# Optimization experiments

Hardware: AMD Instinct MI355X
Metric: run time of the kernel (lower is better)

Reference implementation:

```python
import jax, jax.numpy as jnp
import numpy as np

B, T, D, H, E, K = 8, 1024, 1024, 16, 8, 2
HS = D // H  # head size
LN_EPS = 1e-5


def setup_inputs() -> dict:
    key = jax.random.key(0)
    ks = jax.random.split(key, 12)
    s = 0.02
    return {
        "x":  jax.random.normal(ks[0], (B, T, D), jnp.float32),
        "Wq": jax.random.normal(ks[1], (H, D, HS), jnp.float32) * s,
        "Wk": jax.random.normal(ks[2], (H, D, HS), jnp.float32) * s,
        "Wv": jax.random.normal(ks[3], (H, D, HS), jnp.float32) * s,
        "Wg": jax.random.normal(ks[4], (D, E), jnp.float32) * s,
        "W1": jax.random.normal(ks[5], (E, D, 4 * D), jnp.float32) * s,
        "b1": jnp.zeros((E, 4 * D), jnp.float32),
        "W2": jax.random.normal(ks[6], (E, 4 * D, D), jnp.float32) * s,
        "b2": jnp.zeros((E, D), jnp.float32),
        "g1": jnp.ones((D,), jnp.float32),
        "be1": jnp.zeros((D,), jnp.float32),
        "g2": jnp.ones((D,), jnp.float32),
        "be2": jnp.zeros((D,), jnp.float32),
    }


def _layernorm(h, g, b):
    mu = jnp.mean(h, axis=-1, keepdims=True)
    var = jnp.mean(jnp.square(h - mu), axis=-1, keepdims=True)
    return (h - mu) * jax.lax.rsqrt(var + LN_EPS) * g + b


def _attention(x, Wq, Wk, Wv):
    # per-head projections (no bias)
    q = jnp.einsum('btd,hde->bhte', x, Wq)
    k = jnp.einsum('btd,hde->bhte', x, Wk)
    v = jnp.einsum('btd,hde->bhte', x, Wv)
    # NOTE: original scales by C**-0.5 where C = x.shape[-1] = n_embed
    scores = jnp.einsum('bhte,bhse->bhts', q, k) * (D ** -0.5)
    causal = jnp.tril(jnp.ones((T, T), bool))
    scores = jnp.where(causal, scores, -jnp.inf)
    attn = jax.nn.softmax(scores, axis=-1)  # dropout = identity (eval)
    out = jnp.einsum('bhts,bhse->bhte', attn, v)
    # concat heads: [B,H,T,HS] -> [B,T,H*HS]
    return out.transpose(0, 2, 1, 3).reshape(B, T, D)


def _moe(x, Wg, W1, b1, W2, b2):
    xs = x.reshape(-1, D)                       # [N, D]
    logits = xs @ Wg                            # [N, E]
    w, sel = jax.lax.top_k(logits, K)           # [N, K]
    w = jax.nn.softmax(w.astype(jnp.float32), axis=-1).astype(x.dtype)
    # combine per-token per-expert weight: [N, E]
    we = jnp.sum(w[..., None] * (sel[..., None] == jnp.arange(E)), axis=1)
    res = jnp.zeros_like(xs)
    for e in range(E):  # fixed small expert count
        h = jax.nn.relu(xs @ W1[e] + b1[e])     # [N, 4D]
        y = h @ W2[e] + b2[e]                   # [N, D]
        res = res + we[:, e:e + 1] * y
    return res.reshape(x.shape)


def reference(x, Wq, Wk, Wv, Wg, W1, b1, W2, b2, g1, be1, g2, be2):
    out = x + _layernorm(_attention(x, Wq, Wk, Wv), g1, be1)
    out = out + _layernorm(_moe(x, Wg, W1, b1, W2, b2), g2, be2)
    return out
```

## Files before the change

### kernel.cpp

```cpp
#include <hip/hip_runtime.h>

#define B_    8
#define T_    1024
#define D_    1024
#define H_    16
#define HS_   64
#define E_    8
#define DFF   4096
#define NTOK  8192
#define NROW  16384

typedef unsigned short u16;
typedef unsigned int   u32;
typedef __attribute__((ext_vector_type(8))) short bf8;
typedef __attribute__((ext_vector_type(4))) float f4;

__device__ __forceinline__ u16 f2bf(float f) {
  u32 u = __float_as_uint(f);
  u32 r = (u + 0x7FFFu + ((u >> 16) & 1u)) >> 16;
  return (u16)r;
}
__device__ __forceinline__ float bf2f(u16 h) {
  return __uint_as_float(((u32)h) << 16);
}

__device__ __forceinline__ f4 mfma16(bf8 a, bf8 b, f4 c) {
  return __builtin_amdgcn_mfma_f32_16x16x32_bf16(a, b, c, 0, 0, 0);
}

typedef const __attribute__((address_space(1))) void* gas_ptr;
typedef __attribute__((address_space(3))) void* las_ptr;
__device__ __forceinline__ void async16(const void* g, void* l) {
  __builtin_amdgcn_global_load_lds((gas_ptr)g, (las_ptr)l, 16, 0, 0);
}

__global__ __launch_bounds__(256) void cvt_x_kernel(const float* __restrict__ x,
                                                    u16* __restrict__ xbf) {
  int i = blockIdx.x * 256 + threadIdx.x;
  float4 v = ((const float4*)x)[i];
  ushort4 o;
  o.x = f2bf(v.x); o.y = f2bf(v.y); o.z = f2bf(v.z); o.w = f2bf(v.w);
  ((ushort4*)xbf)[i] = o;
}

__global__ __launch_bounds__(256) void transpose_cvt_kernel(
    const float* __restrict__ src, u16* __restrict__ dst,
    int R, int C, size_t sStride, size_t dStride) {
  __shared__ float t[32][33];
  src += (size_t)blockIdx.z * sStride;
  dst += (size_t)blockIdx.z * dStride;
  int r0 = blockIdx.x * 32, c0 = blockIdx.y * 32;
  int tx = threadIdx.x & 31, ty = threadIdx.x >> 5;
#pragma unroll
  for (int i = 0; i < 32; i += 8)
    t[ty + i][tx] = src[(size_t)(r0 + ty + i) * C + (c0 + tx)];
  __syncthreads();
#pragma unroll
  for (int i = 0; i < 32; i += 8)
    dst[(size_t)(c0 + ty + i) * R + (r0 + tx)] = f2bf(t[tx][ty + i]);
}

__global__ __launch_bounds__(256) void vtrans_kernel(const u16* __restrict__ qkv,
                                                     u16* __restrict__ Vt) {
  __shared__ u16 t[32][33];
  int bh = blockIdx.z, b = bh >> 4, h = bh & 15;
  const u16* Vg = qkv + (size_t)(32 + h) * NTOK * HS_ + (size_t)b * T_ * HS_;
  u16* Vp = Vt + (size_t)bh * HS_ * T_;
  int t0 = blockIdx.x * 32, c0 = blockIdx.y * 32;
  int tx = threadIdx.x & 31, ty = threadIdx.x >> 5;
#pragma unroll
  for (int i = 0; i < 32; i += 8)
    t[ty + i][tx] = Vg[(size_t)(t0 + ty + i) * HS_ + c0 + tx];
  __syncthreads();
#pragma unroll
  for (int i = 0; i < 32; i += 8)
    Vp[(size_t)(c0 + ty + i) * T_ + t0 + tx] = t[tx][ty + i];
}

__global__ __launch_bounds__(256) void gating_kernel(
    const float* __restrict__ x, const float* __restrict__ Wg,
    int* __restrict__ sel, float* __restrict__ wgt) {
  int wave = threadIdx.x >> 6, lane = threadIdx.x & 63;
  int t = blockIdx.x * 4 + wave;
  int e = lane & 7, grp = lane >> 3;
  const float* xr = x + (size_t)t * D_;
  float acc = 0.f;
  for (int i = 0; i < 128; ++i) {
    int d = grp + i * 8;
    acc += xr[d] * Wg[d * 8 + e];
  }
  acc += __shfl_xor(acc, 8);
  acc += __shfl_xor(acc, 16);
  acc += __shfl_xor(acc, 32);
  float lg[8];
#pragma unroll
  for (int j = 0; j < 8; ++j) lg[j] = __shfl(acc, j);
  int s0 = 0; float v0 = lg[0];
#pragma unroll
  for (int j = 1; j < 8; ++j) if (lg[j] > v0) { v0 = lg[j]; s0 = j; }
  int s1 = -1; float v1 = -3.4e38f;
#pragma unroll
  for (int j = 0; j < 8; ++j) if (j != s0 && lg[j] > v1) { v1 = lg[j]; s1 = j; }
  if (lane == 0) {
    float dd = __expf(v1 - v0);
    float w0 = 1.f / (1.f + dd);
    sel[2 * t]     = s0; sel[2 * t + 1] = s1;
    wgt[2 * t]     = w0; wgt[2 * t + 1] = dd * w0;
  }
}

__global__ __launch_bounds__(256) void offsets_kernel(const int* __restrict__ sel,
                                                      int* __restrict__ meta) {
  __shared__ int hist[E_];
  int tid = threadIdx.x;
  if (tid < E_) hist[tid] = 0;
  __syncthreads();
  for (int i = tid; i < NROW; i += 256) atomicAdd(&hist[sel[i]], 1);
  __syncthreads();
  if (tid == 0) {
    int s = 0, mb = 0;
    for (int e = 0; e < E_; ++e) {
      int c = hist[e];
      meta[e] = c; meta[8 + e] = s; meta[16 + e] = mb;
      s += c; mb += (c + 127) >> 7;
    }
    meta[24] = mb;
  }
}

__global__ __launch_bounds__(256) void assign_kernel(
    const int* __restrict__ sel, const float* __restrict__ wgt,
    const int* __restrict__ meta, int* __restrict__ gidx,
    float* __restrict__ gw, int* __restrict__ rowmap) {
  int e = blockIdx.x, tid = threadIdx.x, lane = tid & 63, wv = tid >> 6;
  __shared__ int wsum[4];
  __shared__ int carry;
  if (tid == 0) carry = meta[8 + e];
  __syncthreads();
  for (int base = 0; base < NROW; base += 256) {
    int idx = base + tid;
    int f = (sel[idx] == e) ? 1 : 0;
    unsigned long long mask = __ballot(f);
    int pre = __popcll(mask & ((1ull << lane) - 1ull));
    if (lane == 0) wsum[wv] = __popcll(mask);
    __syncthreads();
    int woff = 0;
    for (int w = 0; w < wv; ++w) woff += wsum[w];
    int cb = carry;
    if (f) {
      int pos = cb + woff + pre;
      gidx[pos] = idx >> 1;
      gw[pos] = wgt[idx];
      rowmap[idx] = pos;
    }
    __syncthreads();
    if (tid == 0) carry = cb + wsum[0] + wsum[1] + wsum[2] + wsum[3];
    __syncthreads();
  }
}

template <int MODE>
__global__ __launch_bounds__(256) void gemm_bt(
    const u16* __restrict__ A, const u16* __restrict__ Bt,
    u16* __restrict__ outB, const float* __restrict__ bias,
    const int* __restrict__ meta, const int* __restrict__ gidx, int K) {
  int n0 = blockIdx.y * 128;
  int n_e = 0, off = 0, m0, e = 0;
  const u16* Ap = A;
  const u16* Bp = Bt;
  if constexpr (MODE != 0) {
    int xb = blockIdx.x;
#pragma unroll
    for (int j = 1; j < 8; ++j) if (meta[16 + j] <= xb) e = j;
    n_e = meta[e];
    off = meta[8 + e];
    m0 = (xb - meta[16 + e]) * 128;
    if (m0 >= n_e) return;
    if constexpr (MODE == 1) {
      Bp = Bt + (size_t)e * DFF * 1024;
    } else {
      Ap = A + (size_t)off * DFF;
      Bp = Bt + (size_t)e * 1024 * DFF;
    }
  } else {
    m0 = blockIdx.x * 128;
  }

  __shared__ __align__(16) u16 As[128 * 64];
  __shared__ __align__(16) u16 Bs[128 * 64];
  int tid = threadIdx.x, lane = tid & 63, wave = tid >> 6;
  int wm = wave >> 1, wn = wave & 1, ml = lane & 15, quad = lane >> 4;
  int lrow = lane >> 3;
  int gcol = ((lane & 7) ^ lrow) * 8;

  const u16* arow[4];
  const u16* brow[4];
#pragma unroll
  for (int r = 0; r < 4; ++r) {
    int row = wave * 32 + r * 8;
    int ra = m0 + row + lrow;
    if constexpr (MODE == 1) {
      int rr = ra < n_e ? ra : n_e - 1;
      arow[r] = Ap + (size_t)gidx[off + rr] * 1024 + gcol;
    } else if constexpr (MODE == 2) {
      int rr = ra < n_e ? ra : n_e - 1;
      arow[r] = Ap + (size_t)rr * DFF + gcol;
    } else {
      arow[r] = Ap + (size_t)ra * 1024 + gcol;
    }
    brow[r] = Bp + (size_t)(n0 + row + lrow) * K + gcol;
  }

  f4 acc[4][4];
#pragma unroll
  for (int i = 0; i < 4; ++i)
#pragma unroll
    for (int j = 0; j < 4; ++j) acc[i][j] = (f4){0.f, 0.f, 0.f, 0.f};

  int mlx = ml & 7;
  for (int k0 = 0; k0 < K; k0 += 64) {
    __syncthreads();
#pragma unroll
    for (int r = 0; r < 4; ++r) {
      int row = wave * 32 + r * 8;
      async16(arow[r] + k0, &As[row * 64]);
      async16(brow[r] + k0, &Bs[row * 64]);
    }
    __syncthreads();
#pragma unroll
    for (int kk = 0; kk < 64; kk += 32) {
      int p = (((kk >> 3) + quad) ^ mlx) * 8;
      bf8 af[4], bfr[4];
#pragma unroll
      for (int mi = 0; mi < 4; ++mi)
        af[mi] = *(const bf8*)&As[(wm * 64 + mi * 16 + ml) * 64 + p];
#pragma unroll
      for (int ni = 0; ni < 4; ++ni)
        bfr[ni] = *(const bf8*)&Bs[(wn * 64 + ni * 16 + ml) * 64 + p];
#pragma unroll
      for (int mi = 0; mi < 4; ++mi)
#pragma unroll
        for (int ni = 0; ni < 4; ++ni)
          acc[mi][ni] = mfma16(af[mi], bfr[ni], acc[mi][ni]);
    }
  }

#pragma unroll
  for (int mi = 0; mi < 4; ++mi)
#pragma unroll
    for (int ni = 0; ni < 4; ++ni)
#pragma unroll
      for (int rg = 0; rg < 4; ++rg) {
        int m = m0 + wm * 64 + mi * 16 + quad * 4 + rg;
        int n = n0 + wn * 64 + ni * 16 + ml;
        float v = acc[mi][ni][rg];
        if constexpr (MODE == 0) {
          int pl = n >> 6, col = n & 63;
          outB[(size_t)pl * NTOK * HS_ + (size_t)m * HS_ + col] = f2bf(v);
        } else if constexpr (MODE == 1) {
          if (m < n_e) {
            float hv = v + bias[e * DFF + n];
            outB[(size_t)(off + m) * DFF + n] = f2bf(fmaxf(hv, 0.f));
          }
        } else {
          if (m < n_e) {
            outB[(size_t)(off + m) * 1024 + n] = f2bf(v + bias[e * 1024 + n]);
          }
        }
      }
}

__global__ __launch_bounds__(256) void attn_kernel(const u16* __restrict__ qkv,
                                                   const u16* __restrict__ Vt,
                                                   float* __restrict__ attn_out) {
  int qt = blockIdx.x, bh = blockIdx.y;
  int b = bh >> 4, h = bh & 15;
  int q0 = qt * 64;
  const u16* Qg = qkv + (size_t)h * NTOK * HS_ + (size_t)b * T_ * HS_;
  const u16* Kg = qkv + (size_t)(16 + h) * NTOK * HS_ + (size_t)b * T_ * HS_;
  const u16* Vp = Vt + (size_t)bh * HS_ * T_;
  __shared__ __align__(16) u16 Qs[64 * 72];
  __shared__ __align__(16) u16 Ks[64 * 72];
  __shared__ __align__(16) u16 Vs[64 * 72];
  __shared__ __align__(16) u16 Ps[64 * 72];
  int tid = threadIdx.x, lane = tid & 63, wave = tid >> 6;
  int ml = lane & 15, quad = lane >> 4;

  for (int i = tid; i < 512; i += 256) {
    int r = i >> 3, c = (i & 7) * 8;
    *(uint4*)&Qs[r * 72 + c] = *(const uint4*)(Qg + (size_t)(q0 + r) * HS_ + c);
  }

  f4 acc_o[4];
  float m_[4], l_[4];
#pragma unroll
  for (int i = 0; i < 4; ++i) {
    acc_o[i] = (f4){0.f, 0.f, 0.f, 0.f};
    m_[i] = -1e30f; l_[i] = 0.f;
  }

  for (int ck = 0; ck <= qt; ++ck) {
    int kv0 = ck * 64;
    __syncthreads();
    for (int i = tid; i < 512; i += 256) {
      int r = i >> 3, c = (i & 7) * 8;
      *(uint4*)&Ks[r * 72 + c] = *(const uint4*)(Kg + (size_t)(kv0 + r) * HS_ + c);
      *(uint4*)&Vs[r * 72 + c] = *(const uint4*)(Vp + (size_t)r * T_ + kv0 + c);
    }
    __syncthreads();

    f4 sacc[4];
#pragma unroll
    for (int nt = 0; nt < 4; ++nt) sacc[nt] = (f4){0.f, 0.f, 0.f, 0.f};
#pragma unroll
    for (int kk = 0; kk < 64; kk += 32) {
      bf8 a = *(const bf8*)&Qs[(wave * 16 + ml) * 72 + kk + quad * 8];
#pragma unroll
      for (int nt = 0; nt < 4; ++nt) {
        bf8 bk = *(const bf8*)&Ks[(nt * 16 + ml) * 72 + kk + quad * 8];
        sacc[nt] = mfma16(a, bk, sacc[nt]);
      }
    }

    bool dm = (kv0 == q0);
    float pv[4][4], mx[4];
#pragma unroll
    for (int rg = 0; rg < 4; ++rg) {
      int gq = q0 + wave * 16 + quad * 4 + rg;
      float mm = -1e30f;
#pragma unroll
      for (int nt = 0; nt < 4; ++nt) {
        float s = sacc[nt][rg] * 0.03125f;
        if (dm && (kv0 + nt * 16 + ml) > gq) s = -1e30f;
        pv[nt][rg] = s;
        mm = fmaxf(mm, s);
      }
      mx[rg] = mm;
    }
#pragma unroll
    for (int off = 1; off < 16; off <<= 1)
#pragma unroll
      for (int rg = 0; rg < 4; ++rg) mx[rg] = fmaxf(mx[rg], __shfl_xor(mx[rg], off));

    float al[4], rs[4];
#pragma unroll
    for (int rg = 0; rg < 4; ++rg) {
      float mn = fmaxf(m_[rg], mx[rg]);
      al[rg] = __expf(m_[rg] - mn);
      m_[rg] = mn;
      float r = 0.f;
#pragma unroll
      for (int nt = 0; nt < 4; ++nt) {
        float ev = __expf(pv[nt][rg] - mn);
        pv[nt][rg] = ev;
        r += ev;
      }
      rs[rg] = r;
    }
#pragma unroll
    for (int off = 1; off < 16; off <<= 1)
#pragma unroll
      for (int rg = 0; rg < 4; ++rg) rs[rg] += __shfl_xor(rs[rg], off);

#pragma unroll
    for (int rg = 0; rg < 4; ++rg) {
      l_[rg] = al[rg] * l_[rg] + rs[rg];
#pragma unroll
      for (int nt = 0; nt < 4; ++nt) {
        acc_o[nt][rg] *= al[rg];
        Ps[(wave * 16 + quad * 4 + rg) * 72 + nt * 16 + ml] = f2bf(pv[nt][rg]);
      }
    }

#pragma unroll
    for (int kk = 0; kk < 64; kk += 32) {
      bf8 a = *(const bf8*)&Ps[(wave * 16 + ml) * 72 + kk + quad * 8];
#pragma unroll
      for (int ci = 0; ci < 4; ++ci) {
        bf8 bv = *(const bf8*)&Vs[(ci * 16 + ml) * 72 + kk + quad * 8];
        acc_o[ci] = mfma16(a, bv, acc_o[ci]);
      }
    }
  }

#pragma unroll
  for (int rg = 0; rg < 4; ++rg) {
    float inv = 1.f / l_[rg];
    int gq = q0 + wave * 16 + quad * 4 + rg;
    float* orow = attn_out + (size_t)(b * T_ + gq) * D_ + h * HS_;
#pragma unroll
    for (int ci = 0; ci < 4; ++ci) orow[ci * 16 + ml] = acc_o[ci][rg] * inv;
  }
}

__global__ __launch_bounds__(256) void final_kernel(
    const float* __restrict__ x, const float* __restrict__ attn,
    const u16* __restrict__ Y, const int* __restrict__ rowmap,
    const float* __restrict__ wgt,
    const float* __restrict__ g1, const float* __restrict__ be1,
    const float* __restrict__ g2, const float* __restrict__ be2,
    float* __restrict__ out) {
  int t = blockIdx.x, tid = threadIdx.x;
  int lane = tid & 63, wave = tid >> 6;
  float4 av = ((const float4*)(attn + (size_t)t * D_))[tid];
  int r0 = rowmap[2 * t], r1 = rowmap[2 * t + 1];
  float w0 = wgt[2 * t], w1 = wgt[2 * t + 1];
  ushort4 y0 = ((const ushort4*)(Y + (size_t)r0 * D_))[tid];
  ushort4 y1 = ((const ushort4*)(Y + (size_t)r1 * D_))[tid];
  float4 mv;
  mv.x = w0 * bf2f(y0.x) + w1 * bf2f(y1.x);
  mv.y = w0 * bf2f(y0.y) + w1 * bf2f(y1.y);
  mv.z = w0 * bf2f(y0.z) + w1 * bf2f(y1.z);
  mv.w = w0 * bf2f(y0.w) + w1 * bf2f(y1.w);

  float sa = av.x + av.y + av.z + av.w;
  float qa = av.x * av.x + av.y * av.y + av.z * av.z + av.w * av.w;
  float sm = mv.x + mv.y + mv.z + mv.w;
  float qm = mv.x * mv.x + mv.y * mv.y + mv.z * mv.z + mv.w * mv.w;
#pragma unroll
  for (int off = 1; off < 64; off <<= 1) {
    sa += __shfl_xor(sa, off);
    qa += __shfl_xor(qa, off);
    sm += __shfl_xor(sm, off);
    qm += __shfl_xor(qm, off);
  }
  __shared__ float red[4][4];
  if (lane == 0) { red[wave][0] = sa; red[wave][1] = qa; red[wave][2] = sm; red[wave][3] = qm; }
  __syncthreads();
  sa = red[0][0] + red[1][0] + red[2][0] + red[3][0];
  qa = red[0][1] + red[1][1] + red[2][1] + red[3][1];
  sm = red[0][2] + red[1][2] + red[2][2] + red[3][2];
  qm = red[0][3] + red[1][3] + red[2][3] + red[3][3];
  const float inv_d = 1.f / 1024.f;
  float mu1 = sa * inv_d, var1 = qa * inv_d - mu1 * mu1;
  float mu2 = sm * inv_d, var2 = qm * inv_d - mu2 * mu2;
  float rs1 = rsqrtf(var1 + 1e-5f), rs2 = rsqrtf(var2 + 1e-5f);

  float4 xv = ((const float4*)(x + (size_t)t * D_))[tid];
  float4 g1v = ((const float4*)g1)[tid], b1v = ((const float4*)be1)[tid];
  float4 g2v = ((const float4*)g2)[tid], b2v = ((const float4*)be2)[tid];
  float4 o;
  o.x = xv.x + (av.x - mu1) * rs1 * g1v.x + b1v.x + (mv.x - mu2) * rs2 * g2v.x + b2v.x;
  o.y = xv.y + (av.y - mu1) * rs1 * g1v.y + b1v.y + (mv.y - mu2) * rs2 * g2v.y + b2v.y;
  o.z = xv.z + (av.z - mu1) * rs1 * g1v.z + b1v.z + (mv.z - mu2) * rs2 * g2v.z + b2v.z;
  o.w = xv.w + (av.w - mu1) * rs1 * g1v.w + b1v.w + (mv.w - mu2) * rs2 * g2v.w + b2v.w;
  ((float4*)(out + (size_t)t * D_))[tid] = o;
}

extern "C" void kernel_launch(void* const* d_in, const int* in_sizes, int n_in,
                              void* d_out, int out_size, void* d_ws, size_t ws_size,
                              hipStream_t stream) {
  const float* x   = (const float*)d_in[0];
  const float* Wq  = (const float*)d_in[1];
  const float* Wk  = (const float*)d_in[2];
  const float* Wv  = (const float*)d_in[3];
  const float* Wg  = (const float*)d_in[4];
  const float* W1  = (const float*)d_in[5];
  const float* b1  = (const float*)d_in[6];
  const float* W2  = (const float*)d_in[7];
  const float* b2  = (const float*)d_in[8];
  const float* g1  = (const float*)d_in[9];
  const float* be1 = (const float*)d_in[10];
  const float* g2  = (const float*)d_in[11];
  const float* be2 = (const float*)d_in[12];
  float* out = (float*)d_out;

  char* ws = (char*)d_ws;
  size_t off = 0;
  auto alloc = [&](size_t bytes) -> void* {
    void* p = ws + off;
    off = (off + bytes + 255) & ~(size_t)255;
    return p;
  };
  u16*   xbf    = (u16*)alloc((size_t)NTOK * D_ * 2);
  u16*   wqkvt  = (u16*)alloc((size_t)48 * 64 * 1024 * 2);
  u16*   w1t    = (u16*)alloc((size_t)E_ * DFF * 1024 * 2);
  u16*   w2t    = (u16*)alloc((size_t)E_ * 1024 * DFF * 2);
  u16*   qkv    = (u16*)alloc((size_t)48 * NTOK * HS_ * 2);
  float* attn   = (float*)alloc((size_t)NTOK * D_ * 4);
  u16*   Hbuf   = (u16*)alloc((size_t)NROW * DFF * 2);
  u16*   Ybuf   = (u16*)alloc((size_t)NROW * 1024 * 2);
  int*   meta   = (int*)alloc(256);
  int*   sel    = (int*)alloc(NROW * 4);
  float* wgt    = (float*)alloc(NROW * 4);
  int*   gidx   = (int*)alloc(NROW * 4);
  float* gw     = (float*)alloc(NROW * 4);
  int*   rowmap = (int*)alloc(NROW * 4);
  u16*   Vt     = Hbuf;
  (void)ws_size; (void)in_sizes; (void)n_in; (void)out_size; (void)gw;

  cvt_x_kernel<<<NTOK * D_ / 1024, 256, 0, stream>>>(x, xbf);
  transpose_cvt_kernel<<<dim3(32, 2, 16), 256, 0, stream>>>(Wq, wqkvt, 1024, 64, 65536, 65536);
  transpose_cvt_kernel<<<dim3(32, 2, 16), 256, 0, stream>>>(Wk, wqkvt + 16 * 65536, 1024, 64, 65536, 65536);
  transpose_cvt_kernel<<<dim3(32, 2, 16), 256, 0, stream>>>(Wv, wqkvt + 32 * 65536, 1024, 64, 65536, 65536);
  transpose_cvt_kernel<<<dim3(32, 128, 8), 256, 0, stream>>>(W1, w1t, 1024, 4096, (size_t)1024 * 4096, (size_t)1024 * 4096);
  transpose_cvt_kernel<<<dim3(128, 32, 8), 256, 0, stream>>>(W2, w2t, 4096, 1024, (size_t)4096 * 1024, (size_t)4096 * 1024);

  gating_kernel<<<NTOK / 4, 256, 0, stream>>>(x, Wg, sel, wgt);
  offsets_kernel<<<1, 256, 0, stream>>>(sel, meta);
  assign_kernel<<<E_, 256, 0, stream>>>(sel, wgt, meta, gidx, gw, rowmap);

  gemm_bt<0><<<dim3(64, 24), 256, 0, stream>>>(xbf, wqkvt, qkv, nullptr, nullptr, nullptr, 1024);
  vtrans_kernel<<<dim3(32, 2, 128), 256, 0, stream>>>(qkv, Vt);
  attn_kernel<<<dim3(16, 128), 256, 0, stream>>>(qkv, Vt, attn);

  gemm_bt<1><<<dim3(136, 32), 256, 0, stream>>>(xbf, w1t, Hbuf, b1, meta, gidx, 1024);
  gemm_bt<2><<<dim3(136, 8), 256, 0, stream>>>(Hbuf, w2t, Ybuf, b2, meta, gidx, 4096);

  final_kernel<<<NTOK, 256, 0, stream>>>(x, attn, Ybuf, rowmap, wgt, g1, be1, g2, be2, out);
}
```

Measured before the change: 1.128 ms.

## Replace 128x128 GEMM with double-buffered 256x256 tile, 8-wave pipelined kernel

The GEMM moves from 128x128 tiles with 4 waves and one LDS buffer to 256x256 tiles with 8 waves and double-buffered LDS. Global-to-LDS async loads for the next k-tile are interleaved with MFMA phases, and s_setprio raises priority during the MFMA bursts. The MoE routing metadata gains 256-row block offsets to match the new tile. This aims to raise data reuse per tile and hide load latency. In exchange, padding waste per expert grows, fewer blocks are launched, and LDS use reaches 128KB per block.

```diff
diff --git a/kernel.cpp b/kernel.cpp
--- a/kernel.cpp
+++ b/kernel.cpp
@@ -32,6 +32,12 @@
 typedef __attribute__((address_space(3))) void* las_ptr;
 __device__ __forceinline__ void async16(const void* g, void* l) {
   __builtin_amdgcn_global_load_lds((gas_ptr)g, (las_ptr)l, 16, 0, 0);
+}
+
+__device__ __forceinline__ void bar() {
+  asm volatile("" ::: "memory");
+  __builtin_amdgcn_s_barrier();
+  asm volatile("" ::: "memory");
 }
 
 __global__ __launch_bounds__(256) void cvt_x_kernel(const float* __restrict__ x,
@@ -118,13 +124,14 @@
   for (int i = tid; i < NROW; i += 256) atomicAdd(&hist[sel[i]], 1);
   __syncthreads();
   if (tid == 0) {
-    int s = 0, mb = 0;
+    int s = 0, mb = 0, mb2 = 0;
     for (int e = 0; e < E_; ++e) {
       int c = hist[e];
-      meta[e] = c; meta[8 + e] = s; meta[16 + e] = mb;
-      s += c; mb += (c + 127) >> 7;
+      meta[e] = c; meta[8 + e] = s; meta[16 + e] = mb; meta[32 + e] = mb2;
+      s += c; mb += (c + 127) >> 7; mb2 += (c + 255) >> 8;
     }
     meta[24] = mb;
+    meta[40] = mb2;
   }
 }
 
@@ -160,21 +167,21 @@
 }
 
 template <int MODE>
-__global__ __launch_bounds__(256) void gemm_bt(
+__global__ __launch_bounds__(512, 2) void gemm256(
     const u16* __restrict__ A, const u16* __restrict__ Bt,
     u16* __restrict__ outB, const float* __restrict__ bias,
     const int* __restrict__ meta, const int* __restrict__ gidx, int K) {
-  int n0 = blockIdx.y * 128;
+  int n0 = blockIdx.y * 256;
   int n_e = 0, off = 0, m0, e = 0;
   const u16* Ap = A;
   const u16* Bp = Bt;
   if constexpr (MODE != 0) {
     int xb = blockIdx.x;
 #pragma unroll
-    for (int j = 1; j < 8; ++j) if (meta[16 + j] <= xb) e = j;
+    for (int j = 1; j < 8; ++j) if (meta[32 + j] <= xb) e = j;
     n_e = meta[e];
     off = meta[8 + e];
-    m0 = (xb - meta[16 + e]) * 128;
+    m0 = (xb - meta[32 + e]) * 256;
     if (m0 >= n_e) return;
     if constexpr (MODE == 1) {
       Bp = Bt + (size_t)e * DFF * 1024;
@@ -183,75 +190,142 @@
       Bp = Bt + (size_t)e * 1024 * DFF;
     }
   } else {
-    m0 = blockIdx.x * 128;
-  }
-
-  __shared__ __align__(16) u16 As[128 * 64];
-  __shared__ __align__(16) u16 Bs[128 * 64];
-  int tid = threadIdx.x, lane = tid & 63, wave = tid >> 6;
-  int wm = wave >> 1, wn = wave & 1, ml = lane & 15, quad = lane >> 4;
+    m0 = blockIdx.x * 256;
+  }
+
+  __shared__ __align__(16) u16 As[2][256 * 64];
+  __shared__ __align__(16) u16 Bs[2][256 * 64];
+
+  int tid = threadIdx.x, lane = tid & 63, w = tid >> 6;
+  int wm = w >> 2, wn = w & 3;
+  int ml = lane & 15, quad = lane >> 4;
   int lrow = lane >> 3;
   int gcol = ((lane & 7) ^ lrow) * 8;
 
-  const u16* arow[4];
-  const u16* brow[4];
-#pragma unroll
-  for (int r = 0; r < 4; ++r) {
-    int row = wave * 32 + r * 8;
-    int ra = m0 + row + lrow;
+  const u16* aptr[4];
+  const u16* bptr[4];
+#pragma unroll
+  for (int i = 0; i < 4; ++i) {
+    int ra = m0 + i * 64 + w * 8 + lrow;
     if constexpr (MODE == 1) {
       int rr = ra < n_e ? ra : n_e - 1;
-      arow[r] = Ap + (size_t)gidx[off + rr] * 1024 + gcol;
+      aptr[i] = Ap + (size_t)gidx[off + rr] * 1024 + gcol;
     } else if constexpr (MODE == 2) {
       int rr = ra < n_e ? ra : n_e - 1;
-      arow[r] = Ap + (size_t)rr * DFF + gcol;
+      aptr[i] = Ap + (size_t)rr * DFF + gcol;
     } else {
-      arow[r] = Ap + (size_t)ra * 1024 + gcol;
-    }
-    brow[r] = Bp + (size_t)(n0 + row + lrow) * K + gcol;
-  }
-
-  f4 acc[4][4];
-#pragma unroll
-  for (int i = 0; i < 4; ++i)
+      aptr[i] = Ap + (size_t)ra * 1024 + gcol;
+    }
+    bptr[i] = Bp + (size_t)(n0 + i * 64 + w * 8 + lrow) * K + gcol;
+  }
+
+  const int NT = K >> 6;
+
+  auto stA = [&](int buf, int t, int h) {
+#pragma unroll
+    for (int j = 0; j < 2; ++j) {
+      int i = h * 2 + j;
+      async16(aptr[i] + t * 64, &As[buf][(i * 64 + w * 8) * 64]);
+    }
+  };
+  auto stB = [&](int buf, int t, int h) {
+#pragma unroll
+    for (int j = 0; j < 2; ++j) {
+      int i = h * 2 + j;
+      async16(bptr[i] + t * 64, &Bs[buf][(i * 64 + w * 8) * 64]);
+    }
+  };
+
+  f4 acc[8][4];
+#pragma unroll
+  for (int i = 0; i < 8; ++i)
 #pragma unroll
     for (int j = 0; j < 4; ++j) acc[i][j] = (f4){0.f, 0.f, 0.f, 0.f};
 
-  int mlx = ml & 7;
-  for (int k0 = 0; k0 < K; k0 += 64) {
-    __syncthreads();
-#pragma unroll
-    for (int r = 0; r < 4; ++r) {
-      int row = wave * 32 + r * 8;
-      async16(arow[r] + k0, &As[row * 64]);
-      async16(brow[r] + k0, &Bs[row * 64]);
-    }
-    __syncthreads();
-#pragma unroll
-    for (int kk = 0; kk < 64; kk += 32) {
-      int p = (((kk >> 3) + quad) ^ mlx) * 8;
-      bf8 af[4], bfr[4];
-#pragma unroll
-      for (int mi = 0; mi < 4; ++mi)
-        af[mi] = *(const bf8*)&As[(wm * 64 + mi * 16 + ml) * 64 + p];
-#pragma unroll
-      for (int ni = 0; ni < 4; ++ni)
-        bfr[ni] = *(const bf8*)&Bs[(wn * 64 + ni * 16 + ml) * 64 + p];
-#pragma unroll
-      for (int mi = 0; mi < 4; ++mi)
-#pragma unroll
-        for (int ni = 0; ni < 4; ++ni)
-          acc[mi][ni] = mfma16(af[mi], bfr[ni], acc[mi][ni]);
-    }
-  }
-
-#pragma unroll
-  for (int mi = 0; mi < 4; ++mi)
+  stA(0, 0, 0); stA(0, 0, 1); stB(0, 0, 0); stB(0, 0, 1);
+  stA(1, 1, 0);
+  asm volatile("s_waitcnt vmcnt(2)" ::: "memory");
+  bar();
+
+  int mq = ml & 7;
+  bf8 af[8], bfr[4];
+
+  for (int t = 0; t < NT; ++t) {
+    const int c = t & 1;
+    const u16* Ac = As[c];
+    const u16* Bc = Bs[c];
+
+#pragma unroll
+    for (int mi = 0; mi < 8; ++mi)
+      af[mi] = *(const bf8*)&Ac[(wm * 128 + mi * 16 + ml) * 64 + ((quad) ^ mq) * 8];
+#pragma unroll
+    for (int ni = 0; ni < 2; ++ni)
+      bfr[ni] = *(const bf8*)&Bc[(wn * 64 + ni * 16 + ml) * 64 + ((quad) ^ mq) * 8];
+    if (t + 1 < NT) stA(c ^ 1, t + 1, 1);
+    bar();
+    __builtin_amdgcn_s_setprio(1);
+#pragma unroll
+    for (int mi = 0; mi < 8; ++mi) {
+      acc[mi][0] = mfma16(af[mi], bfr[0], acc[mi][0]);
+      acc[mi][1] = mfma16(af[mi], bfr[1], acc[mi][1]);
+    }
+    __builtin_amdgcn_s_setprio(0);
+    bar();
+
+#pragma unroll
+    for (int ni = 2; ni < 4; ++ni)
+      bfr[ni] = *(const bf8*)&Bc[(wn * 64 + ni * 16 + ml) * 64 + ((quad) ^ mq) * 8];
+    if (t + 1 < NT) stB(c ^ 1, t + 1, 0);
+    bar();
+    __builtin_amdgcn_s_setprio(1);
+#pragma unroll
+    for (int mi = 0; mi < 8; ++mi) {
+      acc[mi][2] = mfma16(af[mi], bfr[2], acc[mi][2]);
+      acc[mi][3] = mfma16(af[mi], bfr[3], acc[mi][3]);
+    }
+    __builtin_amdgcn_s_setprio(0);
+    bar();
+
+#pragma unroll
+    for (int mi = 0; mi < 8; ++mi)
+      af[mi] = *(const bf8*)&Ac[(wm * 128 + mi * 16 + ml) * 64 + ((4 + quad) ^ mq) * 8];
+#pragma unroll
+    for (int ni = 0; ni < 2; ++ni)
+      bfr[ni] = *(const bf8*)&Bc[(wn * 64 + ni * 16 + ml) * 64 + ((4 + quad) ^ mq) * 8];
+    if (t + 1 < NT) stB(c ^ 1, t + 1, 1);
+    bar();
+    __builtin_amdgcn_s_setprio(1);
+#pragma unroll
+    for (int mi = 0; mi < 8; ++mi) {
+      acc[mi][0] = mfma16(af[mi], bfr[0], acc[mi][0]);
+      acc[mi][1] = mfma16(af[mi], bfr[1], acc[mi][1]);
+    }
+    __builtin_amdgcn_s_setprio(0);
+    bar();
+
+#pragma unroll
+    for (int ni = 2; ni < 4; ++ni)
+      bfr[ni] = *(const bf8*)&Bc[(wn * 64 + ni * 16 + ml) * 64 + ((4 + quad) ^ mq) * 8];
+    if (t + 2 < NT) stA(c, t + 2, 0);
+    bar();
+    __builtin_amdgcn_s_setprio(1);
+#pragma unroll
+    for (int mi = 0; mi < 8; ++mi) {
+      acc[mi][2] = mfma16(af[mi], bfr[2], acc[mi][2]);
+      acc[mi][3] = mfma16(af[mi], bfr[3], acc[mi][3]);
+    }
+    __builtin_amdgcn_s_setprio(0);
+    asm volatile("s_waitcnt vmcnt(2)" ::: "memory");
+    bar();
+  }
+
+#pragma unroll
+  for (int mi = 0; mi < 8; ++mi)
 #pragma unroll
     for (int ni = 0; ni < 4; ++ni)
 #pragma unroll
       for (int rg = 0; rg < 4; ++rg) {
-        int m = m0 + wm * 64 + mi * 16 + quad * 4 + rg;
+        int m = m0 + wm * 128 + mi * 16 + quad * 4 + rg;
         int n = n0 + wn * 64 + ni * 16 + ml;
         float v = acc[mi][ni][rg];
         if constexpr (MODE == 0) {
@@ -500,12 +574,12 @@
   offsets_kernel<<<1, 256, 0, stream>>>(sel, meta);
   assign_kernel<<<E_, 256, 0, stream>>>(sel, wgt, meta, gidx, gw, rowmap);
 
-  gemm_bt<0><<<dim3(64, 24), 256, 0, stream>>>(xbf, wqkvt, qkv, nullptr, nullptr, nullptr, 1024);
+  gemm256<0><<<dim3(32, 12), 512, 0, stream>>>(xbf, wqkvt, qkv, nullptr, nullptr, nullptr, 1024);
   vtrans_kernel<<<dim3(32, 2, 128), 256, 0, stream>>>(qkv, Vt);
   attn_kernel<<<dim3(16, 128), 256, 0, stream>>>(qkv, Vt, attn);
 
-  gemm_bt<1><<<dim3(136, 32), 256, 0, stream>>>(xbf, w1t, Hbuf, b1, meta, gidx, 1024);
-  gemm_bt<2><<<dim3(136, 8), 256, 0, stream>>>(Hbuf, w2t, Ybuf, b2, meta, gidx, 4096);
+  gemm256<1><<<dim3(72, 16), 512, 0, stream>>>(xbf, w1t, Hbuf, b1, meta, gidx, 1024);
+  gemm256<2><<<dim3(72, 4), 512, 0, stream>>>(Hbuf, w2t, Ybuf, b2, meta, gidx, 4096);
 
   final_kernel<<<NTOK, 256, 0, stream>>>(x, attn, Ybuf, rowmap, wgt, g1, be1, g2, be2, out);
 }
```

Result: slower. 1.241 ms (+10.0%).
